# Performance work log

Hardware: AMD Instinct MI355X
Metric: run time of the kernel (lower is better)

Reference implementation:

```python
import jax, jax.numpy as jnp
import numpy as np

G, N, H = 64, 512, 64          # graphs, nodes/graph, hidden
NT = G * N                     # total nodes
DEG = 32
ET = NT * DEG                  # total edges
KP = int(np.ceil(0.7 * N))     # TopKPooling keep per graph (359)
NP2 = G * KP                   # nodes after pooling
F_IN, NC, NA = 128, 2, 6
seg = jax.ops.segment_sum


def graph_norm(h, batch, num_g, w, b, ms, eps=1e-5):
    cnt = seg(jnp.ones((h.shape[0], 1), h.dtype), batch, num_segments=num_g)
    mean = seg(h, batch, num_segments=num_g) / cnt
    hc = h - ms * mean[batch]
    var = seg(hc * hc, batch, num_segments=num_g) / cnt
    return w * hc / jnp.sqrt(var[batch] + eps) + b


def sage(h, src, tgt, valid, Ws, Wn, b, n_nodes):
    # PyG SAGEConv (mean aggr): out_i = x_i@Ws + mean_{j->i} x_j @ Wn + b
    msg = h[src] * valid[:, None]
    agg = seg(msg, tgt, num_segments=n_nodes)
    deg = seg(valid, tgt, num_segments=n_nodes)
    return h @ Ws + (agg / jnp.maximum(deg, 1.0)[:, None]) @ Wn + b


def setup_inputs() -> dict:
    key = jax.random.key(0)
    ks = jax.random.split(key, 20)
    offs = (jnp.arange(G) * N)[:, None]
    src = (jax.random.randint(ks[0], (G, N * DEG), 0, N) + offs).reshape(-1)
    tgt = (jax.random.randint(ks[1], (G, N * DEG), 0, N) + offs).reshape(-1)
    edge_index = jnp.stack([src, tgt])  # within-graph edges

    def lin(k, fi, fo):
        return jax.random.normal(k, (fi, fo), jnp.float32) / np.sqrt(fi)

    return {
        "x": jax.random.normal(ks[2], (NT, F_IN), jnp.float32),
        "edge_index": edge_index,
        "edge_attr": jax.random.uniform(ks[3], (ET,), jnp.float32),
        "coords": jax.random.normal(ks[4], (NT, 3), jnp.float32),
        "anatomical_class": jax.random.randint(ks[5], (NT,), 0, NA),
        "Bk_table": jax.random.normal(ks[6], (NA, H * H), jnp.float32) * 0.05,
        "pos_W": lin(ks[7], 3, H), "pos_b": jnp.zeros((H,), jnp.float32),
        "W1_self": lin(ks[8], F_IN, H), "W1_neigh": lin(ks[9], F_IN, H),
        "b1": jnp.zeros((H,), jnp.float32),
        "gn1_w": jnp.ones((H,), jnp.float32), "gn1_b": jnp.zeros((H,), jnp.float32),
        "gn1_ms": jnp.ones((H,), jnp.float32),
        "pool_p": jax.random.normal(ks[10], (H,), jnp.float32),
        "W2_self": lin(ks[11], H, H), "W2_neigh": lin(ks[12], H, H),
        "b2": jnp.zeros((H,), jnp.float32),
        "gn2_w": jnp.ones((H,), jnp.float32), "gn2_b": jnp.zeros((H,), jnp.float32),
        "gn2_ms": jnp.ones((H,), jnp.float32),
        "lin1_W": lin(ks[13], 3 * H, H), "lin1_b": jnp.zeros((H,), jnp.float32),
        "lin2_W": lin(ks[14], H, NC), "lin2_b": jnp.zeros((NC,), jnp.float32),
    }


def reference(x, edge_index, edge_attr, coords, anatomical_class, Bk_table,
              pos_W, pos_b, W1_self, W1_neigh, b1, gn1_w, gn1_b, gn1_ms,
              pool_p, W2_self, W2_neigh, b2, gn2_w, gn2_b, gn2_ms,
              lin1_W, lin1_b, lin2_W, lin2_b):
    row, col = edge_index[0], edge_index[1]
    batch = jnp.repeat(jnp.arange(G), N)
    # ---- stage 1: anatomical propagation kernel ----
    e = coords @ pos_W + pos_b                                 # [NT, H]
    Ae = seg(edge_attr[:, None] * e[col], row, num_segments=NT)  # SpMM adj @ e
    Bk = Bk_table[anatomical_class].reshape(NT, H, H)
    delta = jnp.einsum('nd,nhd->nh', Ae, Bk)                   # bmm(Ae, Bk^T)
    ones_e = jnp.ones((ET,), x.dtype)
    h = sage(x, row, col, ones_e, W1_self, W1_neigh, b1, NT)
    h = jax.nn.elu(graph_norm(h, batch, G, gn1_w, gn1_b, gn1_ms))
    h = h + delta
    h = jnp.einsum('nij,nj->ni', Bk + delta[:, :, None], h)    # propagate_message
    # ---- TopK pooling (equal-sized graphs) ----
    score = (h @ pool_p) / jnp.linalg.norm(pool_p)
    vals, idx = jax.lax.top_k(score.reshape(G, N), KP)
    perm = (idx + (jnp.arange(G) * N)[:, None]).reshape(-1)    # [NP2]
    h = h[perm] * jnp.tanh(vals).reshape(-1)[:, None]
    batch2 = jnp.repeat(jnp.arange(G), KP)
    node_map = jnp.full((NT,), -1, jnp.int32).at[perm].set(jnp.arange(NP2, dtype=jnp.int32))
    s2, t2 = node_map[row], node_map[col]
    valid = ((s2 >= 0) & (t2 >= 0)).astype(h.dtype)            # masked edge filter
    s2 = jnp.where(s2 >= 0, s2, 0)
    t2 = jnp.where(t2 >= 0, t2, 0)
    # ---- stage 2 ----
    e2 = coords[perm] @ pos_W + pos_b
    Bk2 = Bk_table[anatomical_class[perm]].reshape(NP2, H, H)
    Ae2 = seg(valid[:, None] * e2[t2], s2, num_segments=NP2)   # edge_attr = ones
    delta2 = jnp.einsum('nd,nhd->nh', Ae2, Bk2)
    h = h + delta2
    h = jnp.einsum('nij,nj->ni', Bk2 + delta2[:, :, None], h)
    h = sage(h, s2, t2, valid, W2_self, W2_neigh, b2, NP2)
    h = jax.nn.elu(graph_norm(h, batch2, G, gn2_w, gn2_b, gn2_ms))
    # ---- readout ----
    cnt = seg(jnp.ones((NP2, 1), h.dtype), batch2, num_segments=G)
    hsum = seg(h, batch2, num_segments=G)
    g = jnp.concatenate([hsum / cnt,
                         jax.ops.segment_max(h, batch2, num_segments=G),
                         hsum], axis=1)
    g = jax.nn.relu(g @ lin1_W + lin1_b)
    return jax.nn.log_softmax(g @ lin2_W + lin2_b, axis=1)
```

## Files before the change

kernel.cpp:

```cpp
#include <hip/hip_runtime.h>
#include <math.h>

#define G_    64
#define N_    512
#define H_    64
#define NT_   32768
#define ET_   1048576
#define EPG_  16384
#define KP_   359
#define NP2_  22976
#define FIN_  128
#define ESL_  2048
#define BPB_  (EPG_/ESL_)

__global__ void k_bkT(const float* __restrict__ Bk, float* __restrict__ BkT) {
    int idx = blockIdx.x * 256 + threadIdx.x;
    int c = idx >> 12, r = idx & 4095;
    int h = r >> 6, d = r & 63;
    BkT[c * 4096 + d * 64 + h] = Bk[c * 4096 + h * 64 + d];
}

__global__ void k_pre(const float* __restrict__ Bk, const float* __restrict__ posW,
                      const float* __restrict__ posb, float* __restrict__ PT) {
    int c = blockIdx.x;
    int t = threadIdx.x;
    int i = t >> 6, h = t & 63;
    const float* B = Bk + c * 4096 + h * 64;
    float acc = 0.f;
    for (int d = 0; d < 64; d++) {
        float vd = (i < 3) ? posW[i*64 + d] : posb[d];
        acc += B[d] * vd;
    }
    PT[c*256 + i*64 + h] = acc;
}

__global__ __launch_bounds__(256)
void k_hist(const int* __restrict__ row, const int* __restrict__ col,
            int* __restrict__ histR, int* __restrict__ histC) {
    __shared__ int hr[N_], hc[N_];
    int b = blockIdx.x, g = b >> 3, s = b & (BPB_ - 1);
    int t = threadIdx.x;
    for (int i = t; i < N_; i += 256) { hr[i] = 0; hc[i] = 0; }
    __syncthreads();
    int ebase = g * EPG_ + s * ESL_;
    for (int i = t; i < ESL_; i += 256) {
        atomicAdd(&hr[row[ebase + i] & (N_ - 1)], 1);
        atomicAdd(&hc[col[ebase + i] & (N_ - 1)], 1);
    }
    __syncthreads();
    int nbase = g * N_;
    for (int i = t; i < N_; i += 256) {
        if (hr[i]) atomicAdd(&histR[nbase + i], hr[i]);
        if (hc[i]) atomicAdd(&histC[nbase + i], hc[i]);
    }
}

__global__ __launch_bounds__(256)
void k_scan(int* __restrict__ histR, int* __restrict__ histC,
            int* __restrict__ rowptr, int* __restrict__ colptr,
            float* __restrict__ deg) {
    __shared__ int hr[N_], hc[N_];
    int g = blockIdx.x, t = threadIdx.x;
    int nbase = g * N_;
    for (int i = t; i < N_; i += 256) {
        hr[i] = histR[nbase + i];
        int c = histC[nbase + i];
        hc[i] = c;
        deg[nbase + i] = (float)c;
    }
    __syncthreads();
    int wave = t >> 6, lane = t & 63;
    if (wave < 2) {
        int* h = wave ? hc : hr;
        int base8 = lane * 8;
        int loc[8];
        int tot = 0;
        #pragma unroll
        for (int i = 0; i < 8; i++) { int v = h[base8 + i]; loc[i] = tot; tot += v; }
        int pref = tot;
        for (int off = 1; off < 64; off <<= 1) {
            int u = __shfl_up(pref, off);
            if (lane >= off) pref += u;
        }
        pref -= tot;
        #pragma unroll
        for (int i = 0; i < 8; i++) h[base8 + i] = pref + loc[i];
    }
    __syncthreads();
    int ebase = g * EPG_;
    for (int i = t; i < N_; i += 256) {
        int rp = ebase + hr[i], cp = ebase + hc[i];
        rowptr[nbase + i] = rp;  histR[nbase + i] = rp;
        colptr[nbase + i] = cp;  histC[nbase + i] = cp;
    }
    if (g == 0 && t == 0) { rowptr[NT_] = ET_; colptr[NT_] = ET_; }
}

__global__ __launch_bounds__(256)
void k_scatter(const int* __restrict__ row, const int* __restrict__ col,
               const float* __restrict__ ea,
               int* __restrict__ cursR, int* __restrict__ cursC,
               int2* __restrict__ rowcsr, int* __restrict__ colcsr) {
    int b = blockIdx.x, g = b >> 3, s = b & (BPB_ - 1);
    int t = threadIdx.x;
    int ebase = g * EPG_ + s * ESL_;
    for (int i = t; i < ESL_; i += 256) {
        int rg = row[ebase + i], cg = col[ebase + i];
        float w = ea[ebase + i];
        int pr = atomicAdd(&cursR[rg], 1);
        rowcsr[pr] = make_int2(cg, __float_as_int(w));
        int pc = atomicAdd(&cursC[cg], 1);
        colcsr[pc] = rg;
    }
}

__global__ __launch_bounds__(256)
void k_gemm_dual(const float* __restrict__ in, int K,
                 const float* __restrict__ Wa, const float* __restrict__ Wb,
                 const float* __restrict__ bias, const int* __restrict__ permA,
                 float* __restrict__ outA, float* __restrict__ outB) {
    __shared__ float inT[32 * FIN_];
    int row0 = blockIdx.x * 32;
    int t = threadIdx.x;
    for (int idx = t; idx < 32 * K; idx += 256) inT[idx] = in[row0 * K + idx];
    __syncthreads();
    int c = t & 63, rb = t >> 6;
    const float* ip = inT + (rb * 8) * K;
    float aA[8] = {0,0,0,0,0,0,0,0};
    float aB[8] = {0,0,0,0,0,0,0,0};
    for (int k = 0; k < K; k += 4) {
        float wa0 = Wa[(k+0)*64 + c], wa1 = Wa[(k+1)*64 + c];
        float wa2 = Wa[(k+2)*64 + c], wa3 = Wa[(k+3)*64 + c];
        float wb0 = Wb[(k+0)*64 + c], wb1 = Wb[(k+1)*64 + c];
        float wb2 = Wb[(k+2)*64 + c], wb3 = Wb[(k+3)*64 + c];
        #pragma unroll
        for (int r = 0; r < 8; r++) {
            float4 xv = *(const float4*)&ip[r*K + k];
            aA[r] += xv.x*wa0; aB[r] += xv.x*wb0;
            aA[r] += xv.y*wa1; aB[r] += xv.y*wb1;
            aA[r] += xv.z*wa2; aB[r] += xv.z*wb2;
            aA[r] += xv.w*wa3; aB[r] += xv.w*wb3;
        }
    }
    float bv = bias[c];
    #pragma unroll
    for (int r = 0; r < 8; r++) {
        int node = row0 + rb*8 + r;
        int rowA = permA ? permA[node] : node;
        outA[rowA*64 + c] = aA[r];
        outB[node*64 + c] = aB[r] + bv;
    }
}

__global__ __launch_bounds__(256)
void k_nsum1(const int* __restrict__ rowptr, const int2* __restrict__ rcsr,
             const float* __restrict__ coords, float4* __restrict__ nsum) {
    int node = blockIdx.x * 4 + (threadIdx.x >> 6);
    int lane = threadIdx.x & 63;
    int start = rowptr[node], end = rowptr[node + 1];
    float sx = 0.f, sy = 0.f, sz = 0.f, sw = 0.f;
    for (int k = start + lane; k < end; k += 64) {
        int2 ent = rcsr[k];
        int c = ent.x;
        float w = __int_as_float(ent.y);
        sx += w * coords[c*3+0];
        sy += w * coords[c*3+1];
        sz += w * coords[c*3+2];
        sw += w;
    }
    #pragma unroll
    for (int off = 32; off; off >>= 1) {
        sx += __shfl_xor(sx, off); sy += __shfl_xor(sy, off);
        sz += __shfl_xor(sz, off); sw += __shfl_xor(sw, off);
    }
    if (lane == 0) nsum[node] = make_float4(sx, sy, sz, sw);
}

__global__ __launch_bounds__(256)
void k_gagg(const int* __restrict__ colptr, const int* __restrict__ ccsr,
            const float* __restrict__ y, float* __restrict__ agg) {
    int node = blockIdx.x * 4 + (threadIdx.x >> 6);
    int lane = threadIdx.x & 63;
    int start = colptr[node], end = colptr[node + 1];
    float acc = 0.f;
    #pragma unroll 4
    for (int k = start; k < end; k++) {
        int r = ccsr[k];
        acc += y[r*64 + lane];
    }
    agg[node*64 + lane] = acc;
}

__global__ __launch_bounds__(256)
void k_gnstat(const float* __restrict__ hs, const float* __restrict__ agg,
              const float* __restrict__ deg, float* __restrict__ partial,
              int NPG, int CH, int npc) {
    __shared__ float r1[256], r2[256];
    int b = blockIdx.x;
    int g = b / CH, chunk = b % CH;
    int t = threadIdx.x, c = t & 63, grp = t >> 6;
    int n0 = chunk * npc;
    int nend = min(n0 + npc, NPG);
    float s1 = 0.f, s2 = 0.f;
    for (int n = n0 + grp; n < nend; n += 4) {
        int node = g * NPG + n;
        float v = hs[node*64 + c] + agg[node*64 + c] / fmaxf(deg[node], 1.f);
        s1 += v; s2 += v * v;
    }
    r1[t] = s1; r2[t] = s2;
    __syncthreads();
    if (grp == 0) {
        partial[b*128 + c]      = r1[c] + r1[64+c] + r1[128+c] + r1[192+c];
        partial[b*128 + 64 + c] = r2[c] + r2[64+c] + r2[128+c] + r2[192+c];
    }
}

__global__ void k_gnfin(const float* __restrict__ partial, const float* __restrict__ ms,
                        int CH, int NPG,
                        float* __restrict__ mval, float* __restrict__ istdv) {
    int g = blockIdx.x, t = threadIdx.x;
    float s1 = 0.f, s2 = 0.f;
    for (int i = 0; i < CH; i++) {
        s1 += partial[(g*CH + i)*128 + t];
        s2 += partial[(g*CH + i)*128 + 64 + t];
    }
    float m = s1 / (float)NPG, q = s2 / (float)NPG, msv = ms[t];
    float var = q - msv * m * m * (2.f - msv);
    mval[g*64 + t]  = msv * m;
    istdv[g*64 + t] = rsqrtf(var + 1e-5f);
}

__global__ __launch_bounds__(256)
void k_gnprop(const float* __restrict__ hself, const float* __restrict__ agg,
              const float* __restrict__ deg,
              const float* __restrict__ mval, const float* __restrict__ istdv,
              const float* __restrict__ w, const float* __restrict__ b,
              const float4* __restrict__ nsum, const int* __restrict__ cls,
              const float* __restrict__ PT, const float* __restrict__ BkT,
              float* __restrict__ out) {
    __shared__ float hT[256];
    int t = threadIdx.x;
    int node = blockIdx.x * 4 + (t >> 6);
    int lane = t & 63;
    int g = node >> 9;
    float4 s4 = nsum[node];
    int c = cls[node];
    const float* P = PT + c * 256;
    float d = s4.x*P[lane] + s4.y*P[64+lane] + s4.z*P[128+lane] + s4.w*P[192+lane];
    float v = hself[node*64 + lane] + agg[node*64 + lane] / fmaxf(deg[node], 1.f);
    v = w[lane] * (v - mval[g*64 + lane]) * istdv[g*64 + lane] + b[lane];
    v = v > 0.f ? v : expm1f(v);
    v += d;
    hT[t] = v;
    __syncthreads();
    float ssum = v;
    #pragma unroll
    for (int off = 32; off; off >>= 1) ssum += __shfl_xor(ssum, off);
    const float* B  = BkT + c * 4096;
    const float* hv = hT + (t & ~63);
    float acc = 0.f;
    #pragma unroll 8
    for (int j = 0; j < 64; j++) acc += B[j*64 + lane] * hv[j];
    out[node*64 + lane] = acc + d * ssum;
}

__global__ void k_topk(const float* __restrict__ hp, const float* __restrict__ p,
                       const int* __restrict__ cls,
                       int* __restrict__ perm, float* __restrict__ tanhv,
                       int* __restrict__ node_map, int* __restrict__ class2) {
    __shared__ float key[N_];
    __shared__ int   idxS[N_];
    __shared__ float pS[64];
    __shared__ float nrm;
    int g = blockIdx.x, t = threadIdx.x;
    if (t < 64) pS[t] = p[t];
    __syncthreads();
    if (t == 0) {
        float s = 0.f;
        for (int i = 0; i < 64; i++) s += pS[i] * pS[i];
        nrm = sqrtf(s);
    }
    __syncthreads();
    {
        float acc = 0.f;
        const float* hv = hp + (size_t)(g*N_ + t) * 64;
        for (int cdx = 0; cdx < 64; cdx++) acc += hv[cdx] * pS[cdx];
        key[t]  = acc / nrm;
        idxS[t] = t;
    }
    __syncthreads();
    for (int k = 2; k <= N_; k <<= 1) {
        for (int j = k >> 1; j > 0; j >>= 1) {
            int i = t, ixj = i ^ j;
            if (ixj > i) {
                float ki = key[i], kj = key[ixj];
                int   ii = idxS[i], ij = idxS[ixj];
                bool before = (ki > kj) || (ki == kj && ii < ij);
                bool dir = ((i & k) == 0);
                if (dir ? !before : before) {
                    key[i] = kj; key[ixj] = ki;
                    idxS[i] = ij; idxS[ixj] = ii;
                }
            }
            __syncthreads();
        }
    }
    if (t < KP_) {
        int orig  = idxS[t];
        int gnode = g * N_ + orig;
        int pj    = g * KP_ + t;
        perm[pj]     = gnode;
        tanhv[pj]    = tanhf(key[t]);
        node_map[gnode] = pj;
        class2[pj]   = cls[gnode];
    }
}

__global__ __launch_bounds__(256)
void k_s2pre(const int* __restrict__ rowptr, const int2* __restrict__ rcsr,
             const int* __restrict__ colptr, const int* __restrict__ ccsr,
             const int* __restrict__ perm, const int* __restrict__ nmap,
             const float* __restrict__ coords,
             float4* __restrict__ nsum2, float* __restrict__ deg2) {
    int j = blockIdx.x * 4 + (threadIdx.x >> 6);
    int lane = threadIdx.x & 63;
    int orig = perm[j];
    int start = rowptr[orig], end = rowptr[orig + 1];
    float sx = 0.f, sy = 0.f, sz = 0.f, sw = 0.f;
    for (int k = start + lane; k < end; k += 64) {
        int c = rcsr[k].x;
        if (nmap[c] >= 0) {
            sx += coords[c*3+0]; sy += coords[c*3+1]; sz += coords[c*3+2];
            sw += 1.f;
        }
    }
    int cs = colptr[orig], ce = colptr[orig + 1];
    float dg = 0.f;
    for (int k = cs + lane; k < ce; k += 64) {
        if (nmap[ccsr[k]] >= 0) dg += 1.f;
    }
    #pragma unroll
    for (int off = 32; off; off >>= 1) {
        sx += __shfl_xor(sx, off); sy += __shfl_xor(sy, off);
        sz += __shfl_xor(sz, off); sw += __shfl_xor(sw, off);
        dg += __shfl_xor(dg, off);
    }
    if (lane == 0) { nsum2[j] = make_float4(sx, sy, sz, sw); deg2[j] = dg; }
}

__global__ __launch_bounds__(256)
void k_prop2v(const float* __restrict__ hp, const int* __restrict__ perm,
              const float* __restrict__ tanhv,
              const float4* __restrict__ nsum2, const int* __restrict__ cls2,
              const float* __restrict__ PT, const float* __restrict__ BkT,
              float* __restrict__ out) {
    __shared__ float hT[256];
    int t = threadIdx.x;
    int j = blockIdx.x * 4 + (t >> 6);
    int lane = t & 63;
    int orig = perm[j];
    float tv = tanhv[j];
    float4 s4 = nsum2[j];
    int c = cls2[j];
    const float* P = PT + c * 256;
    float d = s4.x*P[lane] + s4.y*P[64+lane] + s4.z*P[128+lane] + s4.w*P[192+lane];
    float v = hp[orig*64 + lane] * tv + d;
    hT[t] = v;
    __syncthreads();
    float ssum = v;
    #pragma unroll
    for (int off = 32; off; off >>= 1) ssum += __shfl_xor(ssum, off);
    const float* B  = BkT + c * 4096;
    const float* hv = hT + (t & ~63);
    float acc = 0.f;
    #pragma unroll 8
    for (int jj = 0; jj < 64; jj++) acc += B[jj*64 + lane] * hv[jj];
    out[j*64 + lane] = acc + d * ssum;
}

__global__ __launch_bounds__(256)
void k_gagg2(const int* __restrict__ colptr, const int* __restrict__ ccsr,
             const int* __restrict__ perm, const float* __restrict__ y2full,
             float* __restrict__ agg2) {
    int j = blockIdx.x * 4 + (threadIdx.x >> 6);
    int lane = threadIdx.x & 63;
    int orig = perm[j];
    int start = colptr[orig], end = colptr[orig + 1];
    float acc = 0.f;
    #pragma unroll 4
    for (int k = start; k < end; k++) {
        int r = ccsr[k];
        acc += y2full[r*64 + lane];
    }
    agg2[j*64 + lane] = acc;
}

__global__ __launch_bounds__(256)
void k_gnrd(const float* __restrict__ hs, const float* __restrict__ agg,
            const float* __restrict__ deg2,
            const float* __restrict__ mval, const float* __restrict__ istdv,
            const float* __restrict__ w, const float* __restrict__ b,
            float* __restrict__ part, int CH, int npc) {
    __shared__ float r1[256], r2[256];
    int blk = blockIdx.x;
    int g = blk / CH, chunk = blk % CH;
    int t = threadIdx.x, c = t & 63, grp = t >> 6;
    int n0 = chunk * npc, nend = min(n0 + npc, KP_);
    float mv = mval[g*64 + c], is = istdv[g*64 + c], wv = w[c], bv = b[c];
    float s = 0.f, m = -1e30f;
    for (int n = n0 + grp; n < nend; n += 4) {
        int node = g * KP_ + n;
        float v = hs[node*64 + c] + agg[node*64 + c] / fmaxf(deg2[node], 1.f);
        v = wv * (v - mv) * is + bv;
        v = v > 0.f ? v : expm1f(v);
        s += v; m = fmaxf(m, v);
    }
    r1[t] = s; r2[t] = m;
    __syncthreads();
    if (grp == 0) {
        part[blk*128 + c]      = r1[c] + r1[64+c] + r1[128+c] + r1[192+c];
        part[blk*128 + 64 + c] = fmaxf(fmaxf(r2[c], r2[64+c]), fmaxf(r2[128+c], r2[192+c]));
    }
}

__global__ void k_rfin(const float* __restrict__ part, int CH,
                       const float* __restrict__ l1W, const float* __restrict__ l1b,
                       const float* __restrict__ l2W, const float* __restrict__ l2b,
                       float* __restrict__ out) {
    __shared__ float gv[192], rS[64];
    int g = blockIdx.x, t = threadIdx.x;
    float s = 0.f, m = -1e30f;
    for (int i = 0; i < CH; i++) {
        s += part[(g*CH + i)*128 + t];
        m = fmaxf(m, part[(g*CH + i)*128 + 64 + t]);
    }
    gv[t] = s / (float)KP_;
    gv[64 + t] = m;
    gv[128 + t] = s;
    __syncthreads();
    float acc = l1b[t];
    for (int k = 0; k < 192; k++) acc += gv[k] * l1W[k*64 + t];
    rS[t] = fmaxf(acc, 0.f);
    __syncthreads();
    if (t == 0) {
        float l0 = l2b[0], l1v = l2b[1];
        for (int hh = 0; hh < 64; hh++) { l0 += rS[hh]*l2W[hh*2+0]; l1v += rS[hh]*l2W[hh*2+1]; }
        float mx  = fmaxf(l0, l1v);
        float lse = mx + logf(expf(l0 - mx) + expf(l1v - mx));
        out[g*2 + 0] = l0  - lse;
        out[g*2 + 1] = l1v - lse;
    }
}

extern "C" void kernel_launch(void* const* d_in, const int* in_sizes, int n_in,
                              void* d_out, int out_size, void* d_ws, size_t ws_size,
                              hipStream_t stream) {
    const float* x      = (const float*)d_in[0];
    const int*   eidx   = (const int*)  d_in[1];
    const float* eattr  = (const float*)d_in[2];
    const float* coords = (const float*)d_in[3];
    const int*   acls   = (const int*)  d_in[4];
    const float* BkTab  = (const float*)d_in[5];
    const float* posW   = (const float*)d_in[6];
    const float* posb   = (const float*)d_in[7];
    const float* W1s    = (const float*)d_in[8];
    const float* W1n    = (const float*)d_in[9];
    const float* b1     = (const float*)d_in[10];
    const float* gn1w   = (const float*)d_in[11];
    const float* gn1b   = (const float*)d_in[12];
    const float* gn1ms  = (const float*)d_in[13];
    const float* poolp  = (const float*)d_in[14];
    const float* W2s    = (const float*)d_in[15];
    const float* W2n    = (const float*)d_in[16];
    const float* b2     = (const float*)d_in[17];
    const float* gn2w   = (const float*)d_in[18];
    const float* gn2b   = (const float*)d_in[19];
    const float* gn2ms  = (const float*)d_in[20];
    const float* l1W    = (const float*)d_in[21];
    const float* l1b    = (const float*)d_in[22];
    const float* l2W    = (const float*)d_in[23];
    const float* l2b    = (const float*)d_in[24];

    const int* row  = eidx;
    const int* colp = eidx + ET_;

    float* W = (float*)d_ws;
    const size_t NTH = (size_t)NT_ * 64;
    float* b0    = W;
    float* b1buf = W + 1*NTH;
    float* b2buf = W + 2*NTH;
    float* b3buf = W + 3*NTH;
    float* p = W + 4*NTH;
    int2*  rowcsr = (int2*)p;        p += 2*(size_t)ET_;
    int*   colcsr = (int*)p;         p += ET_;
    int*   rowptr = (int*)p;         p += NT_ + 8;
    int*   colptr = (int*)p;         p += NT_ + 8;
    int*   histR  = (int*)p;         p += NT_;
    int*   histC  = (int*)p;         p += NT_;
    float* deg    = p;               p += NT_;
    float* deg2   = p;               p += NP2_;
    float* tanhv  = p;               p += NP2_;
    int*   perm   = (int*)p;         p += NP2_;
    int*   nmap   = (int*)p;         p += NT_;
    int*   cls2   = (int*)p;         p += NP2_;
    float* BkT    = p;               p += 6 * 4096;
    float* PT     = p;               p += 6 * 256;
    float* meanv  = p;               p += G_ * 64;
    float* istdv  = p;               p += G_ * 64;
    float* partial= (float*)histR;
    float4* nsum  = (float4*)b3buf;
    float4* nsum2 = (float4*)b3buf;

    hipMemsetAsync(histR, 0, 2 * NT_ * sizeof(int), stream);
    hipMemsetAsync(nmap, 0xFF, NT_ * sizeof(int), stream);
    k_bkT      <<<96,       256, 0, stream>>>(BkTab, BkT);
    k_pre      <<<6,        256, 0, stream>>>(BkTab, posW, posb, PT);
    k_hist     <<<G_*BPB_,  256, 0, stream>>>(row, colp, histR, histC);
    k_scan     <<<G_,       256, 0, stream>>>(histR, histC, rowptr, colptr, deg);
    k_scatter  <<<G_*BPB_,  256, 0, stream>>>(row, colp, eattr, histR, histC,
                                              rowcsr, colcsr);

    k_gemm_dual<<<NT_/32,  256, 0, stream>>>(x, FIN_, W1n, W1s, b1, nullptr,
                                             b0 , b1buf );
    k_nsum1    <<<NT_/4,   256, 0, stream>>>(rowptr, rowcsr, coords, nsum);
    k_gagg     <<<NT_/4,   256, 0, stream>>>(colptr, colcsr, b0 , b2buf );
    k_gnstat   <<<G_*8,    256, 0, stream>>>(b1buf , b2buf , deg,
                                             partial, N_, 8, 64);
    k_gnfin    <<<G_,      64,  0, stream>>>(partial, gn1ms, 8, N_, meanv, istdv);
    k_gnprop   <<<NT_/4,   256, 0, stream>>>(b1buf , b2buf , deg,
                                             meanv, istdv, gn1w, gn1b,
                                             nsum, acls, PT, BkT,
                                             b1buf );
    k_topk     <<<G_,      512, 0, stream>>>(b1buf , poolp, acls,
                                             perm, tanhv, nmap, cls2);

    k_s2pre    <<<NP2_/4,  256, 0, stream>>>(rowptr, rowcsr, colptr, colcsr,
                                             perm, nmap, coords, nsum2, deg2);
    k_prop2v   <<<NP2_/4,  256, 0, stream>>>(b1buf , perm, tanhv,
                                             nsum2, cls2, PT, BkT, b2buf );
    hipMemsetAsync(b0, 0, NTH * sizeof(float), stream);
    k_gemm_dual<<<NP2_/32, 256, 0, stream>>>(b2buf , 64, W2n, W2s, b2, perm,
                                             b0 , b3buf );
    k_gagg2    <<<NP2_/4,  256, 0, stream>>>(colptr, colcsr, perm, b0 ,
                                             b1buf );
    k_gnstat   <<<G_*6,    256, 0, stream>>>(b3buf , b1buf , deg2,
                                             partial, KP_, 6, 60);
    k_gnfin    <<<G_,      64,  0, stream>>>(partial, gn2ms, 6, KP_, meanv, istdv);
    k_gnrd     <<<G_*6,    256, 0, stream>>>(b3buf , b1buf , deg2,
                                             meanv, istdv, gn2w, gn2b,
                                             partial, 6, 60);
    k_rfin     <<<G_,      64,  0, stream>>>(partial, 6, l1W, l1b, l2W, l2b,
                                             (float*)d_out);
}
```

Baseline: 404.4 us.

## Drop row CSR; build col CSR per graph and compute neighbor sums via shared atomics

Removes the row-CSR construction entirely and replaces the global histogram/scan/scatter pipeline with one 1024-thread block per graph that builds the column CSR in shared memory. The coordinate neighbor sums for both stages are now computed by streaming the raw edge list with shared-memory float atomics per graph, instead of walking row-CSR lists. The two small prep kernels are merged, the nmap memset is folded into the build kernel, and the gather loops are unrolled further. The goal is to cut global atomics, launches and CSR memory traffic, at the cost of low-parallelism per-graph blocks (64 blocks) and nondeterministic float summation order.

Measured after the change: 465.8 us. 1.15x slower.

```diff
diff --git a/kernel.cpp b/kernel.cpp
--- a/kernel.cpp
+++ b/kernel.cpp
@@ -10,108 +10,119 @@
 #define KP_   359
 #define NP2_  22976
 #define FIN_  128
-#define ESL_  2048
-#define BPB_  (EPG_/ESL_)
-
-__global__ void k_bkT(const float* __restrict__ Bk, float* __restrict__ BkT) {
-    int idx = blockIdx.x * 256 + threadIdx.x;
-    int c = idx >> 12, r = idx & 4095;
-    int h = r >> 6, d = r & 63;
-    BkT[c * 4096 + d * 64 + h] = Bk[c * 4096 + h * 64 + d];
-}
-
-__global__ void k_pre(const float* __restrict__ Bk, const float* __restrict__ posW,
-                      const float* __restrict__ posb, float* __restrict__ PT) {
-    int c = blockIdx.x;
-    int t = threadIdx.x;
-    int i = t >> 6, h = t & 63;
-    const float* B = Bk + c * 4096 + h * 64;
-    float acc = 0.f;
-    for (int d = 0; d < 64; d++) {
-        float vd = (i < 3) ? posW[i*64 + d] : posb[d];
-        acc += B[d] * vd;
-    }
-    PT[c*256 + i*64 + h] = acc;
-}
-
-__global__ __launch_bounds__(256)
-void k_hist(const int* __restrict__ row, const int* __restrict__ col,
-            int* __restrict__ histR, int* __restrict__ histC) {
-    __shared__ int hr[N_], hc[N_];
-    int b = blockIdx.x, g = b >> 3, s = b & (BPB_ - 1);
-    int t = threadIdx.x;
-    for (int i = t; i < N_; i += 256) { hr[i] = 0; hc[i] = 0; }
-    __syncthreads();
-    int ebase = g * EPG_ + s * ESL_;
-    for (int i = t; i < ESL_; i += 256) {
-        atomicAdd(&hr[row[ebase + i] & (N_ - 1)], 1);
+
+__global__ void k_prep(const float* __restrict__ Bk, const float* __restrict__ posW,
+                       const float* __restrict__ posb,
+                       float* __restrict__ BkT, float* __restrict__ PT) {
+    int b = blockIdx.x, t = threadIdx.x;
+    if (b < 96) {
+        int idx = b * 256 + t;
+        int c = idx >> 12, r = idx & 4095;
+        int h = r >> 6, d = r & 63;
+        BkT[c * 4096 + d * 64 + h] = Bk[c * 4096 + h * 64 + d];
+    } else {
+        int c = b - 96;
+        int i = t >> 6, h = t & 63;
+        const float* B = Bk + c * 4096 + h * 64;
+        float acc = 0.f;
+        for (int d = 0; d < 64; d++) {
+            float vd = (i < 3) ? posW[i*64 + d] : posb[d];
+            acc += B[d] * vd;
+        }
+        PT[c*256 + i*64 + h] = acc;
+    }
+}
+
+__global__ __launch_bounds__(1024)
+void k_buildc(const int* __restrict__ row, const int* __restrict__ col,
+              int* __restrict__ colptr, int* __restrict__ colcsr,
+              float* __restrict__ deg, int* __restrict__ nmap) {
+    __shared__ int hc[N_];
+    int g = blockIdx.x, t = threadIdx.x;
+    int nbase = g * N_, ebase = g * EPG_;
+    if (t < N_) { hc[t] = 0; nmap[nbase + t] = -1; }
+    __syncthreads();
+    for (int i = t; i < EPG_; i += 1024)
         atomicAdd(&hc[col[ebase + i] & (N_ - 1)], 1);
-    }
-    __syncthreads();
-    int nbase = g * N_;
-    for (int i = t; i < N_; i += 256) {
-        if (hr[i]) atomicAdd(&histR[nbase + i], hr[i]);
-        if (hc[i]) atomicAdd(&histC[nbase + i], hc[i]);
-    }
-}
-
-__global__ __launch_bounds__(256)
-void k_scan(int* __restrict__ histR, int* __restrict__ histC,
-            int* __restrict__ rowptr, int* __restrict__ colptr,
-            float* __restrict__ deg) {
-    __shared__ int hr[N_], hc[N_];
-    int g = blockIdx.x, t = threadIdx.x;
-    int nbase = g * N_;
-    for (int i = t; i < N_; i += 256) {
-        hr[i] = histR[nbase + i];
-        int c = histC[nbase + i];
-        hc[i] = c;
-        deg[nbase + i] = (float)c;
-    }
-    __syncthreads();
-    int wave = t >> 6, lane = t & 63;
-    if (wave < 2) {
-        int* h = wave ? hc : hr;
-        int base8 = lane * 8;
+    __syncthreads();
+    if (t < N_) deg[nbase + t] = (float)hc[t];
+    __syncthreads();
+    if (t < 64) {
+        int base8 = t * 8;
         int loc[8];
         int tot = 0;
         #pragma unroll
-        for (int i = 0; i < 8; i++) { int v = h[base8 + i]; loc[i] = tot; tot += v; }
+        for (int i = 0; i < 8; i++) { int v = hc[base8 + i]; loc[i] = tot; tot += v; }
         int pref = tot;
         for (int off = 1; off < 64; off <<= 1) {
             int u = __shfl_up(pref, off);
-            if (lane >= off) pref += u;
+            if ((t & 63) >= off) pref += u;
         }
         pref -= tot;
         #pragma unroll
-        for (int i = 0; i < 8; i++) h[base8 + i] = pref + loc[i];
-    }
-    __syncthreads();
-    int ebase = g * EPG_;
-    for (int i = t; i < N_; i += 256) {
-        int rp = ebase + hr[i], cp = ebase + hc[i];
-        rowptr[nbase + i] = rp;  histR[nbase + i] = rp;
-        colptr[nbase + i] = cp;  histC[nbase + i] = cp;
-    }
-    if (g == 0 && t == 0) { rowptr[NT_] = ET_; colptr[NT_] = ET_; }
-}
-
-__global__ __launch_bounds__(256)
-void k_scatter(const int* __restrict__ row, const int* __restrict__ col,
-               const float* __restrict__ ea,
-               int* __restrict__ cursR, int* __restrict__ cursC,
-               int2* __restrict__ rowcsr, int* __restrict__ colcsr) {
-    int b = blockIdx.x, g = b >> 3, s = b & (BPB_ - 1);
-    int t = threadIdx.x;
-    int ebase = g * EPG_ + s * ESL_;
-    for (int i = t; i < ESL_; i += 256) {
+        for (int i = 0; i < 8; i++) hc[base8 + i] = pref + loc[i];
+    }
+    __syncthreads();
+    if (t < N_) colptr[nbase + t] = ebase + hc[t];
+    if (g == 0 && t == 0) colptr[NT_] = ET_;
+    __syncthreads();
+    for (int i = t; i < EPG_; i += 1024) {
+        int cg = col[ebase + i], rg = row[ebase + i];
+        int pc = atomicAdd(&hc[cg & (N_ - 1)], 1);
+        colcsr[ebase + pc] = rg;
+    }
+}
+
+__global__ __launch_bounds__(1024)
+void k_nsum1s(const int* __restrict__ row, const int* __restrict__ col,
+              const float* __restrict__ ea, const float* __restrict__ coords,
+              float4* __restrict__ nsum) {
+    __shared__ float tile[N_ * 4];
+    int g = blockIdx.x, t = threadIdx.x;
+    int nbase = g * N_, ebase = g * EPG_;
+    for (int i = t; i < N_ * 4; i += 1024) tile[i] = 0.f;
+    __syncthreads();
+    for (int i = t; i < EPG_; i += 1024) {
+        int rg = row[ebase + i] & (N_ - 1);
+        int cg = col[ebase + i];
+        float w = ea[ebase + i];
+        atomicAdd(&tile[rg*4 + 0], w * coords[cg*3 + 0]);
+        atomicAdd(&tile[rg*4 + 1], w * coords[cg*3 + 1]);
+        atomicAdd(&tile[rg*4 + 2], w * coords[cg*3 + 2]);
+        atomicAdd(&tile[rg*4 + 3], w);
+    }
+    __syncthreads();
+    float* out = (float*)&nsum[nbase];
+    for (int i = t; i < N_ * 4; i += 1024) out[i] = tile[i];
+}
+
+__global__ __launch_bounds__(1024)
+void k_s2pres(const int* __restrict__ row, const int* __restrict__ col,
+              const int* __restrict__ nmap, const float* __restrict__ coords,
+              float4* __restrict__ nsum2, float* __restrict__ deg2) {
+    __shared__ float tile[KP_ * 4];
+    __shared__ float dg[KP_];
+    int g = blockIdx.x, t = threadIdx.x;
+    int pbase = g * KP_, ebase = g * EPG_;
+    for (int i = t; i < KP_ * 4; i += 1024) tile[i] = 0.f;
+    if (t < KP_) dg[t] = 0.f;
+    __syncthreads();
+    for (int i = t; i < EPG_; i += 1024) {
         int rg = row[ebase + i], cg = col[ebase + i];
-        float w = ea[ebase + i];
-        int pr = atomicAdd(&cursR[rg], 1);
-        rowcsr[pr] = make_int2(cg, __float_as_int(w));
-        int pc = atomicAdd(&cursC[cg], 1);
-        colcsr[pc] = rg;
-    }
+        int mr = nmap[rg], mc = nmap[cg];
+        if ((mr | mc) >= 0) {
+            int lr = mr - pbase;
+            atomicAdd(&tile[lr*4 + 0], coords[cg*3 + 0]);
+            atomicAdd(&tile[lr*4 + 1], coords[cg*3 + 1]);
+            atomicAdd(&tile[lr*4 + 2], coords[cg*3 + 2]);
+            atomicAdd(&tile[lr*4 + 3], 1.f);
+            atomicAdd(&dg[mc - pbase], 1.f);
+        }
+    }
+    __syncthreads();
+    float* out = (float*)&nsum2[pbase];
+    for (int i = t; i < KP_ * 4; i += 1024) out[i] = tile[i];
+    if (t < KP_) deg2[pbase + t] = dg[t];
 }
 
 __global__ __launch_bounds__(256)
@@ -153,37 +164,13 @@
 }
 
 __global__ __launch_bounds__(256)
-void k_nsum1(const int* __restrict__ rowptr, const int2* __restrict__ rcsr,
-             const float* __restrict__ coords, float4* __restrict__ nsum) {
-    int node = blockIdx.x * 4 + (threadIdx.x >> 6);
-    int lane = threadIdx.x & 63;
-    int start = rowptr[node], end = rowptr[node + 1];
-    float sx = 0.f, sy = 0.f, sz = 0.f, sw = 0.f;
-    for (int k = start + lane; k < end; k += 64) {
-        int2 ent = rcsr[k];
-        int c = ent.x;
-        float w = __int_as_float(ent.y);
-        sx += w * coords[c*3+0];
-        sy += w * coords[c*3+1];
-        sz += w * coords[c*3+2];
-        sw += w;
-    }
-    #pragma unroll
-    for (int off = 32; off; off >>= 1) {
-        sx += __shfl_xor(sx, off); sy += __shfl_xor(sy, off);
-        sz += __shfl_xor(sz, off); sw += __shfl_xor(sw, off);
-    }
-    if (lane == 0) nsum[node] = make_float4(sx, sy, sz, sw);
-}
-
-__global__ __launch_bounds__(256)
 void k_gagg(const int* __restrict__ colptr, const int* __restrict__ ccsr,
             const float* __restrict__ y, float* __restrict__ agg) {
     int node = blockIdx.x * 4 + (threadIdx.x >> 6);
     int lane = threadIdx.x & 63;
     int start = colptr[node], end = colptr[node + 1];
     float acc = 0.f;
-    #pragma unroll 4
+    #pragma unroll 8
     for (int k = start; k < end; k++) {
         int r = ccsr[k];
         acc += y[r*64 + lane];
@@ -317,38 +304,6 @@
 }
 
 __global__ __launch_bounds__(256)
-void k_s2pre(const int* __restrict__ rowptr, const int2* __restrict__ rcsr,
-             const int* __restrict__ colptr, const int* __restrict__ ccsr,
-             const int* __restrict__ perm, const int* __restrict__ nmap,
-             const float* __restrict__ coords,
-             float4* __restrict__ nsum2, float* __restrict__ deg2) {
-    int j = blockIdx.x * 4 + (threadIdx.x >> 6);
-    int lane = threadIdx.x & 63;
-    int orig = perm[j];
-    int start = rowptr[orig], end = rowptr[orig + 1];
-    float sx = 0.f, sy = 0.f, sz = 0.f, sw = 0.f;
-    for (int k = start + lane; k < end; k += 64) {
-        int c = rcsr[k].x;
-        if (nmap[c] >= 0) {
-            sx += coords[c*3+0]; sy += coords[c*3+1]; sz += coords[c*3+2];
-            sw += 1.f;
-        }
-    }
-    int cs = colptr[orig], ce = colptr[orig + 1];
-    float dg = 0.f;
-    for (int k = cs + lane; k < ce; k += 64) {
-        if (nmap[ccsr[k]] >= 0) dg += 1.f;
-    }
-    #pragma unroll
-    for (int off = 32; off; off >>= 1) {
-        sx += __shfl_xor(sx, off); sy += __shfl_xor(sy, off);
-        sz += __shfl_xor(sz, off); sw += __shfl_xor(sw, off);
-        dg += __shfl_xor(dg, off);
-    }
-    if (lane == 0) { nsum2[j] = make_float4(sx, sy, sz, sw); deg2[j] = dg; }
-}
-
-__global__ __launch_bounds__(256)
 void k_prop2v(const float* __restrict__ hp, const int* __restrict__ perm,
               const float* __restrict__ tanhv,
               const float4* __restrict__ nsum2, const int* __restrict__ cls2,
@@ -387,7 +342,7 @@
     int orig = perm[j];
     int start = colptr[orig], end = colptr[orig + 1];
     float acc = 0.f;
-    #pragma unroll 4
+    #pragma unroll 8
     for (int k = start; k < end; k++) {
         int r = ccsr[k];
         acc += y2full[r*64 + lane];
@@ -491,12 +446,8 @@
     float* b2buf = W + 2*NTH;
     float* b3buf = W + 3*NTH;
     float* p = W + 4*NTH;
-    int2*  rowcsr = (int2*)p;        p += 2*(size_t)ET_;
     int*   colcsr = (int*)p;         p += ET_;
-    int*   rowptr = (int*)p;         p += NT_ + 8;
     int*   colptr = (int*)p;         p += NT_ + 8;
-    int*   histR  = (int*)p;         p += NT_;
-    int*   histC  = (int*)p;         p += NT_;
     float* deg    = p;               p += NT_;
     float* deg2   = p;               p += NP2_;
     float* tanhv  = p;               p += NP2_;
@@ -507,22 +458,16 @@
     float* PT     = p;               p += 6 * 256;
     float* meanv  = p;               p += G_ * 64;
     float* istdv  = p;               p += G_ * 64;
-    float* partial= (float*)histR;
+    float* partial= p;               p += (size_t)G_ * 8 * 128;
     float4* nsum  = (float4*)b3buf;
     float4* nsum2 = (float4*)b3buf;
 
-    hipMemsetAsync(histR, 0, 2 * NT_ * sizeof(int), stream);
-    hipMemsetAsync(nmap, 0xFF, NT_ * sizeof(int), stream);
-    k_bkT      <<<96,       256, 0, stream>>>(BkTab, BkT);
-    k_pre      <<<6,        256, 0, stream>>>(BkTab, posW, posb, PT);
-    k_hist     <<<G_*BPB_,  256, 0, stream>>>(row, colp, histR, histC);
-    k_scan     <<<G_,       256, 0, stream>>>(histR, histC, rowptr, colptr, deg);
-    k_scatter  <<<G_*BPB_,  256, 0, stream>>>(row, colp, eattr, histR, histC,
-                                              rowcsr, colcsr);
+    k_prep     <<<102,     256,  0, stream>>>(BkTab, posW, posb, BkT, PT);
+    k_buildc   <<<G_,      1024, 0, stream>>>(row, colp, colptr, colcsr, deg, nmap);
 
     k_gemm_dual<<<NT_/32,  256, 0, stream>>>(x, FIN_, W1n, W1s, b1, nullptr,
                                              b0 , b1buf );
-    k_nsum1    <<<NT_/4,   256, 0, stream>>>(rowptr, rowcsr, coords, nsum);
+    k_nsum1s   <<<G_,      1024, 0, stream>>>(row, colp, eattr, coords, nsum);
     k_gagg     <<<NT_/4,   256, 0, stream>>>(colptr, colcsr, b0 , b2buf );
     k_gnstat   <<<G_*8,    256, 0, stream>>>(b1buf , b2buf , deg,
                                              partial, N_, 8, 64);
@@ -534,8 +479,7 @@
     k_topk     <<<G_,      512, 0, stream>>>(b1buf , poolp, acls,
                                              perm, tanhv, nmap, cls2);
 
-    k_s2pre    <<<NP2_/4,  256, 0, stream>>>(rowptr, rowcsr, colptr, colcsr,
-                                             perm, nmap, coords, nsum2, deg2);
+    k_s2pres   <<<G_,      1024, 0, stream>>>(row, colp, nmap, coords, nsum2, deg2);
     k_prop2v   <<<NP2_/4,  256, 0, stream>>>(b1buf , perm, tanhv,
                                              nsum2, cls2, PT, BkT, b2buf );
     hipMemsetAsync(b0, 0, NTH * sizeof(float), stream);
```

## Fuse CSR histogram, scan and scatter into one per-graph kernel

Applied to the files above, without the earlier changes.

Replaces the separate histogram, scan and scatter kernels, plus two memsets, with a single 1024-thread block per graph. That block builds the row and column CSR using shared-memory counters and cursors, and it also initializes nmap. The BkT transpose and PT precompute are merged into one launch. Gather loop unroll goes from 4 to 8. The aim is to cut launch and memset overhead and global atomics, at the cost of only 64 blocks doing all CSR construction, which lowers parallelism.

New measurement: 372.0 us. -8.0%, faster.

```diff
diff --git a/kernel.cpp b/kernel.cpp
--- a/kernel.cpp
+++ b/kernel.cpp
@@ -10,64 +10,46 @@
 #define KP_   359
 #define NP2_  22976
 #define FIN_  128
-#define ESL_  2048
-#define BPB_  (EPG_/ESL_)
-
-__global__ void k_bkT(const float* __restrict__ Bk, float* __restrict__ BkT) {
-    int idx = blockIdx.x * 256 + threadIdx.x;
-    int c = idx >> 12, r = idx & 4095;
-    int h = r >> 6, d = r & 63;
-    BkT[c * 4096 + d * 64 + h] = Bk[c * 4096 + h * 64 + d];
-}
-
-__global__ void k_pre(const float* __restrict__ Bk, const float* __restrict__ posW,
-                      const float* __restrict__ posb, float* __restrict__ PT) {
-    int c = blockIdx.x;
-    int t = threadIdx.x;
-    int i = t >> 6, h = t & 63;
-    const float* B = Bk + c * 4096 + h * 64;
-    float acc = 0.f;
-    for (int d = 0; d < 64; d++) {
-        float vd = (i < 3) ? posW[i*64 + d] : posb[d];
-        acc += B[d] * vd;
-    }
-    PT[c*256 + i*64 + h] = acc;
-}
-
-__global__ __launch_bounds__(256)
-void k_hist(const int* __restrict__ row, const int* __restrict__ col,
-            int* __restrict__ histR, int* __restrict__ histC) {
+
+__global__ void k_prep(const float* __restrict__ Bk, const float* __restrict__ posW,
+                       const float* __restrict__ posb,
+                       float* __restrict__ BkT, float* __restrict__ PT) {
+    int b = blockIdx.x, t = threadIdx.x;
+    if (b < 96) {
+        int idx = b * 256 + t;
+        int c = idx >> 12, r = idx & 4095;
+        int h = r >> 6, d = r & 63;
+        BkT[c * 4096 + d * 64 + h] = Bk[c * 4096 + h * 64 + d];
+    } else {
+        int c = b - 96;
+        int i = t >> 6, h = t & 63;
+        const float* B = Bk + c * 4096 + h * 64;
+        float acc = 0.f;
+        for (int d = 0; d < 64; d++) {
+            float vd = (i < 3) ? posW[i*64 + d] : posb[d];
+            acc += B[d] * vd;
+        }
+        PT[c*256 + i*64 + h] = acc;
+    }
+}
+
+__global__ __launch_bounds__(1024)
+void k_build2(const int* __restrict__ row, const int* __restrict__ col,
+              const float* __restrict__ ea,
+              int* __restrict__ rowptr, int* __restrict__ colptr,
+              int2* __restrict__ rowcsr, int* __restrict__ colcsr,
+              float* __restrict__ deg, int* __restrict__ nmap) {
     __shared__ int hr[N_], hc[N_];
-    int b = blockIdx.x, g = b >> 3, s = b & (BPB_ - 1);
-    int t = threadIdx.x;
-    for (int i = t; i < N_; i += 256) { hr[i] = 0; hc[i] = 0; }
-    __syncthreads();
-    int ebase = g * EPG_ + s * ESL_;
-    for (int i = t; i < ESL_; i += 256) {
+    int g = blockIdx.x, t = threadIdx.x;
+    int nbase = g * N_, ebase = g * EPG_;
+    if (t < N_) { hr[t] = 0; hc[t] = 0; nmap[nbase + t] = -1; }
+    __syncthreads();
+    for (int i = t; i < EPG_; i += 1024) {
         atomicAdd(&hr[row[ebase + i] & (N_ - 1)], 1);
         atomicAdd(&hc[col[ebase + i] & (N_ - 1)], 1);
     }
     __syncthreads();
-    int nbase = g * N_;
-    for (int i = t; i < N_; i += 256) {
-        if (hr[i]) atomicAdd(&histR[nbase + i], hr[i]);
-        if (hc[i]) atomicAdd(&histC[nbase + i], hc[i]);
-    }
-}
-
-__global__ __launch_bounds__(256)
-void k_scan(int* __restrict__ histR, int* __restrict__ histC,
-            int* __restrict__ rowptr, int* __restrict__ colptr,
-            float* __restrict__ deg) {
-    __shared__ int hr[N_], hc[N_];
-    int g = blockIdx.x, t = threadIdx.x;
-    int nbase = g * N_;
-    for (int i = t; i < N_; i += 256) {
-        hr[i] = histR[nbase + i];
-        int c = histC[nbase + i];
-        hc[i] = c;
-        deg[nbase + i] = (float)c;
-    }
+    if (t < N_) deg[nbase + t] = (float)hc[t];
     __syncthreads();
     int wave = t >> 6, lane = t & 63;
     if (wave < 2) {
@@ -87,31 +69,76 @@
         for (int i = 0; i < 8; i++) h[base8 + i] = pref + loc[i];
     }
     __syncthreads();
-    int ebase = g * EPG_;
-    for (int i = t; i < N_; i += 256) {
-        int rp = ebase + hr[i], cp = ebase + hc[i];
-        rowptr[nbase + i] = rp;  histR[nbase + i] = rp;
-        colptr[nbase + i] = cp;  histC[nbase + i] = cp;
+    if (t < N_) {
+        rowptr[nbase + t] = ebase + hr[t];
+        colptr[nbase + t] = ebase + hc[t];
     }
     if (g == 0 && t == 0) { rowptr[NT_] = ET_; colptr[NT_] = ET_; }
-}
-
-__global__ __launch_bounds__(256)
-void k_scatter(const int* __restrict__ row, const int* __restrict__ col,
-               const float* __restrict__ ea,
-               int* __restrict__ cursR, int* __restrict__ cursC,
-               int2* __restrict__ rowcsr, int* __restrict__ colcsr) {
-    int b = blockIdx.x, g = b >> 3, s = b & (BPB_ - 1);
-    int t = threadIdx.x;
-    int ebase = g * EPG_ + s * ESL_;
-    for (int i = t; i < ESL_; i += 256) {
+    __syncthreads();
+    for (int i = t; i < EPG_; i += 1024) {
         int rg = row[ebase + i], cg = col[ebase + i];
         float w = ea[ebase + i];
-        int pr = atomicAdd(&cursR[rg], 1);
-        rowcsr[pr] = make_int2(cg, __float_as_int(w));
-        int pc = atomicAdd(&cursC[cg], 1);
-        colcsr[pc] = rg;
-    }
+        int pr = atomicAdd(&hr[rg & (N_ - 1)], 1);
+        rowcsr[ebase + pr] = make_int2(cg, __float_as_int(w));
+        int pc = atomicAdd(&hc[cg & (N_ - 1)], 1);
+        colcsr[ebase + pc] = rg;
+    }
+}
+
+__global__ __launch_bounds__(256)
+void k_nsum1(const int* __restrict__ rowptr, const int2* __restrict__ rcsr,
+             const float* __restrict__ coords, float4* __restrict__ nsum) {
+    int node = blockIdx.x * 4 + (threadIdx.x >> 6);
+    int lane = threadIdx.x & 63;
+    int start = rowptr[node], end = rowptr[node + 1];
+    float sx = 0.f, sy = 0.f, sz = 0.f, sw = 0.f;
+    for (int k = start + lane; k < end; k += 64) {
+        int2 ent = rcsr[k];
+        int c = ent.x;
+        float w = __int_as_float(ent.y);
+        sx += w * coords[c*3+0];
+        sy += w * coords[c*3+1];
+        sz += w * coords[c*3+2];
+        sw += w;
+    }
+    #pragma unroll
+    for (int off = 32; off; off >>= 1) {
+        sx += __shfl_xor(sx, off); sy += __shfl_xor(sy, off);
+        sz += __shfl_xor(sz, off); sw += __shfl_xor(sw, off);
+    }
+    if (lane == 0) nsum[node] = make_float4(sx, sy, sz, sw);
+}
+
+__global__ __launch_bounds__(256)
+void k_s2pre(const int* __restrict__ rowptr, const int2* __restrict__ rcsr,
+             const int* __restrict__ colptr, const int* __restrict__ ccsr,
+             const int* __restrict__ perm, const int* __restrict__ nmap,
+             const float* __restrict__ coords,
+             float4* __restrict__ nsum2, float* __restrict__ deg2) {
+    int j = blockIdx.x * 4 + (threadIdx.x >> 6);
+    int lane = threadIdx.x & 63;
+    int orig = perm[j];
+    int start = rowptr[orig], end = rowptr[orig + 1];
+    float sx = 0.f, sy = 0.f, sz = 0.f, sw = 0.f;
+    for (int k = start + lane; k < end; k += 64) {
+        int c = rcsr[k].x;
+        if (nmap[c] >= 0) {
+            sx += coords[c*3+0]; sy += coords[c*3+1]; sz += coords[c*3+2];
+            sw += 1.f;
+        }
+    }
+    int cs = colptr[orig], ce = colptr[orig + 1];
+    float dg = 0.f;
+    for (int k = cs + lane; k < ce; k += 64) {
+        if (nmap[ccsr[k]] >= 0) dg += 1.f;
+    }
+    #pragma unroll
+    for (int off = 32; off; off >>= 1) {
+        sx += __shfl_xor(sx, off); sy += __shfl_xor(sy, off);
+        sz += __shfl_xor(sz, off); sw += __shfl_xor(sw, off);
+        dg += __shfl_xor(dg, off);
+    }
+    if (lane == 0) { nsum2[j] = make_float4(sx, sy, sz, sw); deg2[j] = dg; }
 }
 
 __global__ __launch_bounds__(256)
@@ -153,37 +180,13 @@
 }
 
 __global__ __launch_bounds__(256)
-void k_nsum1(const int* __restrict__ rowptr, const int2* __restrict__ rcsr,
-             const float* __restrict__ coords, float4* __restrict__ nsum) {
-    int node = blockIdx.x * 4 + (threadIdx.x >> 6);
-    int lane = threadIdx.x & 63;
-    int start = rowptr[node], end = rowptr[node + 1];
-    float sx = 0.f, sy = 0.f, sz = 0.f, sw = 0.f;
-    for (int k = start + lane; k < end; k += 64) {
-        int2 ent = rcsr[k];
-        int c = ent.x;
-        float w = __int_as_float(ent.y);
-        sx += w * coords[c*3+0];
-        sy += w * coords[c*3+1];
-        sz += w * coords[c*3+2];
-        sw += w;
-    }
-    #pragma unroll
-    for (int off = 32; off; off >>= 1) {
-        sx += __shfl_xor(sx, off); sy += __shfl_xor(sy, off);
-        sz += __shfl_xor(sz, off); sw += __shfl_xor(sw, off);
-    }
-    if (lane == 0) nsum[node] = make_float4(sx, sy, sz, sw);
-}
-
-__global__ __launch_bounds__(256)
 void k_gagg(const int* __restrict__ colptr, const int* __restrict__ ccsr,
             const float* __restrict__ y, float* __restrict__ agg) {
     int node = blockIdx.x * 4 + (threadIdx.x >> 6);
     int lane = threadIdx.x & 63;
     int start = colptr[node], end = colptr[node + 1];
     float acc = 0.f;
-    #pragma unroll 4
+    #pragma unroll 8
     for (int k = start; k < end; k++) {
         int r = ccsr[k];
         acc += y[r*64 + lane];
@@ -317,38 +320,6 @@
 }
 
 __global__ __launch_bounds__(256)
-void k_s2pre(const int* __restrict__ rowptr, const int2* __restrict__ rcsr,
-             const int* __restrict__ colptr, const int* __restrict__ ccsr,
-             const int* __restrict__ perm, const int* __restrict__ nmap,
-             const float* __restrict__ coords,
-             float4* __restrict__ nsum2, float* __restrict__ deg2) {
-    int j = blockIdx.x * 4 + (threadIdx.x >> 6);
-    int lane = threadIdx.x & 63;
-    int orig = perm[j];
-    int start = rowptr[orig], end = rowptr[orig + 1];
-    float sx = 0.f, sy = 0.f, sz = 0.f, sw = 0.f;
-    for (int k = start + lane; k < end; k += 64) {
-        int c = rcsr[k].x;
-        if (nmap[c] >= 0) {
-            sx += coords[c*3+0]; sy += coords[c*3+1]; sz += coords[c*3+2];
-            sw += 1.f;
-        }
-    }
-    int cs = colptr[orig], ce = colptr[orig + 1];
-    float dg = 0.f;
-    for (int k = cs + lane; k < ce; k += 64) {
-        if (nmap[ccsr[k]] >= 0) dg += 1.f;
-    }
-    #pragma unroll
-    for (int off = 32; off; off >>= 1) {
-        sx += __shfl_xor(sx, off); sy += __shfl_xor(sy, off);
-        sz += __shfl_xor(sz, off); sw += __shfl_xor(sw, off);
-        dg += __shfl_xor(dg, off);
-    }
-    if (lane == 0) { nsum2[j] = make_float4(sx, sy, sz, sw); deg2[j] = dg; }
-}
-
-__global__ __launch_bounds__(256)
 void k_prop2v(const float* __restrict__ hp, const int* __restrict__ perm,
               const float* __restrict__ tanhv,
               const float4* __restrict__ nsum2, const int* __restrict__ cls2,
@@ -387,7 +358,7 @@
     int orig = perm[j];
     int start = colptr[orig], end = colptr[orig + 1];
     float acc = 0.f;
-    #pragma unroll 4
+    #pragma unroll 8
     for (int k = start; k < end; k++) {
         int r = ccsr[k];
         acc += y2full[r*64 + lane];
@@ -495,8 +466,6 @@
     int*   colcsr = (int*)p;         p += ET_;
     int*   rowptr = (int*)p;         p += NT_ + 8;
     int*   colptr = (int*)p;         p += NT_ + 8;
-    int*   histR  = (int*)p;         p += NT_;
-    int*   histC  = (int*)p;         p += NT_;
     float* deg    = p;               p += NT_;
     float* deg2   = p;               p += NP2_;
     float* tanhv  = p;               p += NP2_;
@@ -507,18 +476,13 @@
     float* PT     = p;               p += 6 * 256;
     float* meanv  = p;               p += G_ * 64;
     float* istdv  = p;               p += G_ * 64;
-    float* partial= (float*)histR;
+    float* partial= p;               p += (size_t)G_ * 8 * 128;
     float4* nsum  = (float4*)b3buf;
     float4* nsum2 = (float4*)b3buf;
 
-    hipMemsetAsync(histR, 0, 2 * NT_ * sizeof(int), stream);
-    hipMemsetAsync(nmap, 0xFF, NT_ * sizeof(int), stream);
-    k_bkT      <<<96,       256, 0, stream>>>(BkTab, BkT);
-    k_pre      <<<6,        256, 0, stream>>>(BkTab, posW, posb, PT);
-    k_hist     <<<G_*BPB_,  256, 0, stream>>>(row, colp, histR, histC);
-    k_scan     <<<G_,       256, 0, stream>>>(histR, histC, rowptr, colptr, deg);
-    k_scatter  <<<G_*BPB_,  256, 0, stream>>>(row, colp, eattr, histR, histC,
-                                              rowcsr, colcsr);
+    k_prep     <<<102,     256,  0, stream>>>(BkTab, posW, posb, BkT, PT);
+    k_build2   <<<G_,      1024, 0, stream>>>(row, colp, eattr, rowptr, colptr,
+                                              rowcsr, colcsr, deg, nmap);
 
     k_gemm_dual<<<NT_/32,  256, 0, stream>>>(x, FIN_, W1n, W1s, b1, nullptr,
                                              b0 , b1buf );
```
